# Kernel optimization log

Hardware: AMD Instinct MI355X
Metric: run time of the kernel (lower is better)

## Reference

```python
import jax, jax.numpy as jnp
import numpy as np

N_CH = 128      # n_channels (out_channels)
MID = 128       # mid_channels
NF = 16         # num_filters
N_NODES = 50000


def _omeg():
    i = jnp.arange(NF, dtype=jnp.float32)
    return (10.0 * N_CH ** (1.0 - 2.0 * i / NF)).reshape(1, NF)


def setup_inputs() -> dict:
    key = jax.random.key(0)
    ks = jax.random.split(key, 16)
    E = 800000
    inp = {
        "x": jax.random.normal(ks[0], (N_NODES, N_CH), jnp.float32),
        "edge_index": jax.random.randint(ks[1], (2, E), 0, N_NODES, jnp.int64),
        "edge_attr": jax.random.normal(ks[2], (E, N_CH), jnp.float32),
        "x_pos": jax.random.normal(ks[3], (N_NODES, 3), jnp.float32),
    }
    def lin(k, fan_in, fan_out):
        kw, kb = jax.random.split(k)
        bound = 1.0 / np.sqrt(fan_in)
        w = jax.random.uniform(kw, (fan_in, fan_out), jnp.float32, -bound, bound)
        b = jax.random.uniform(kb, (fan_out,), jnp.float32, -bound, bound)
        return w, b
    inp["w1"], inp["b1"] = lin(ks[4], N_CH, N_CH)          # atomwise1
    inp["mw1"], inp["mb1"] = lin(ks[5], 2 * NF + 2 * N_CH, MID)  # message MLP
    inp["mw2"], inp["mb2"] = lin(ks[6], MID, MID)
    inp["mw3"], inp["mb3"] = lin(ks[7], MID, N_CH)
    inp["w2"], inp["b2"] = lin(ks[8], N_CH, N_CH)          # atomwise2
    inp["w3"], inp["b3"] = lin(ks[9], N_CH, N_CH)          # atomwise3
    return inp


def reference(x, edge_index, edge_attr, x_pos, w1, b1, mw1, mb1, mw2, mb2, mw3, mb3, w2, b2, w3, b3):
    h = x @ w1 + b1                                   # atomwise1 [N, C]
    src, dst = edge_index[0], edge_index[1]           # PyG: x_j = src, x_i = dst
    r = jnp.linalg.norm(x_pos[dst] - x_pos[src], axis=-1, keepdims=True)  # [E,1], p=2
    feat = r * _omeg()                                # [E, NF]
    msg_in = jnp.concatenate([jnp.sin(feat), jnp.cos(feat), edge_attr, h[src]], axis=-1)
    m = jax.nn.gelu(msg_in @ mw1 + mb1, approximate=False)
    m = jax.nn.gelu(m @ mw2 + mb2, approximate=False)
    m = m @ mw3 + mb3                                 # dropout is identity at eval
    agg = jax.ops.segment_sum(m, dst, num_segments=N_NODES)
    h = h + agg                                       # residual in cfconv
    out = jax.nn.relu(h @ w2 + b2) @ w3 + b3
    return out
```

## Files before the change

kernel.cpp:

```cpp
#include <hip/hip_runtime.h>
#include <math.h>

#define NCH 128
#define TE 64
#define TF 32
#define AP 296
#define WP 40
#define XP 136

typedef __attribute__((ext_vector_type(8))) _Float16 half8;
typedef __attribute__((ext_vector_type(4))) _Float16 half4;
typedef __attribute__((ext_vector_type(4))) float f32x4;

__device__ __forceinline__ float gelu_exact(float v) {
    return 0.5f * v * (1.0f + erff(v * 0.70710678118654752f));
}

__device__ __forceinline__ void sincos_rev(float rev, float* s, float* c) {
    float fr = rev - floorf(rev);
#if __has_builtin(__builtin_amdgcn_sinf) && __has_builtin(__builtin_amdgcn_cosf)
    *s = __builtin_amdgcn_sinf(fr);
    *c = __builtin_amdgcn_cosf(fr);
#else
    float rad = fr * 6.283185307179586f;
    *s = sinf(rad);
    *c = cosf(rad);
#endif
}

__global__ __launch_bounds__(256) void k_prep(const float* __restrict__ W,
                                              _Float16* __restrict__ out, int total) {
    int idx = blockIdx.x * 256 + threadIdx.x;
    if (idx >= total) return;
    int k = idx >> 7, n = idx & 127;
    out[(size_t)(k >> 5) * 4096 + n * 32 + (k & 31)] = (_Float16)W[idx];
}

__global__ __launch_bounds__(256) void k_prep_frag(const float* __restrict__ W,
                                                   _Float16* __restrict__ out,
                                                   int nchunks) {
    int idx = blockIdx.x * 256 + threadIdx.x;
    if (idx >= nchunks * 512) return;
    int c    = idx >> 9;
    int r    = idx & 511;
    int wv   = r >> 7;
    int nf   = (r >> 6) & 1;
    int lane = r & 63;
    int n  = wv * 32 + nf * 16 + (lane & 15);
    int k0 = c * 32 + (lane >> 4) * 8;
    half8 v;
    #pragma unroll
    for (int j = 0; j < 8; ++j) v[j] = (_Float16)W[(size_t)(k0 + j) * NCH + n];
    *(half8*)(out + (size_t)idx * 8) = v;
}

__global__ __launch_bounds__(256, 4) void k_aw1_mfma(
    const float* __restrict__ x, const _Float16* __restrict__ wc,
    const float* __restrict__ b1, float* __restrict__ h,
    _Float16* __restrict__ h2, int N)
{
    __shared__ __align__(16) _Float16 Xs[64][XP];
    __shared__ __align__(16) _Float16 Ws[128][WP];

    const int tid  = threadIdx.x;
    const int row0 = blockIdx.x * 64;
    const int lane = tid & 63;
    const int w    = tid >> 6;
    const int lrow = lane & 15;
    const int lk8  = lane >> 4;
    const int n0   = w * 32;

    const uint4* wsrc = (const uint4*)wc;
    uint4 pv0 = wsrc[tid], pv1 = wsrc[tid + 256];

    #pragma unroll
    for (int t = 0; t < 8; ++t) {
        int idx = tid + t * 256;
        int r = idx >> 5, f4 = idx & 31;
        int gr = row0 + r;
        float4 v = {0.f, 0.f, 0.f, 0.f};
        if (gr < N) v = *(const float4*)(x + (size_t)gr * NCH + f4 * 4);
        half4 p = {(_Float16)v.x, (_Float16)v.y, (_Float16)v.z, (_Float16)v.w};
        *(half4*)&Xs[r][f4 * 4] = p;
    }
    *(uint4*)&Ws[tid >> 2][(tid & 3) * 8]        = pv0;
    *(uint4*)&Ws[64 + (tid >> 2)][(tid & 3) * 8] = pv1;
    __syncthreads();

    f32x4 acc[4][2];
    #pragma unroll
    for (int mb = 0; mb < 4; ++mb)
        #pragma unroll
        for (int nf = 0; nf < 2; ++nf) acc[mb][nf] = (f32x4){0.f, 0.f, 0.f, 0.f};

    for (int i = 0; i < 4; ++i) {
        if (i < 3) {
            const uint4* s = (const uint4*)(wc + (i + 1) * 4096);
            pv0 = s[tid]; pv1 = s[tid + 256];
        }
        half8 av[4], bv[2];
        #pragma unroll
        for (int mb = 0; mb < 4; ++mb)
            av[mb] = *(const half8*)&Xs[mb * 16 + lrow][i * 32 + lk8 * 8];
        #pragma unroll
        for (int nf = 0; nf < 2; ++nf)
            bv[nf] = *(const half8*)&Ws[n0 + nf * 16 + lrow][lk8 * 8];
        #pragma unroll
        for (int mb = 0; mb < 4; ++mb)
            #pragma unroll
            for (int nf = 0; nf < 2; ++nf)
                acc[mb][nf] = __builtin_amdgcn_mfma_f32_16x16x32_f16(
                    av[mb], bv[nf], acc[mb][nf], 0, 0, 0);
        __syncthreads();
        if (i < 3) {
            *(uint4*)&Ws[tid >> 2][(tid & 3) * 8]        = pv0;
            *(uint4*)&Ws[64 + (tid >> 2)][(tid & 3) * 8] = pv1;
        }
        __syncthreads();
    }

    float bi0 = b1[n0 + lrow], bi1 = b1[n0 + 16 + lrow];
    #pragma unroll
    for (int mb = 0; mb < 4; ++mb)
        #pragma unroll
        for (int q = 0; q < 4; ++q) {
            int gr = row0 + mb * 16 + lk8 * 4 + q;
            if (gr < N) {
                float v0 = acc[mb][0][q] + bi0;
                float v1 = acc[mb][1][q] + bi1;
                h[(size_t)gr * NCH + n0 + lrow]       = v0;
                h[(size_t)gr * NCH + n0 + 16 + lrow]  = v1;
                h2[(size_t)gr * NCH + n0 + lrow]      = (_Float16)v0;
                h2[(size_t)gr * NCH + n0 + 16 + lrow] = (_Float16)v1;
            }
        }
}

__global__ __launch_bounds__(256, 8) void k_edges_mfma(
    const int* __restrict__ ei, const float* __restrict__ eattr,
    const float* __restrict__ xpos, const _Float16* __restrict__ h2,
    float* h,
    const _Float16* __restrict__ wf,
    const float* __restrict__ mb1, const float* __restrict__ mb2,
    const float* __restrict__ mb3, int E)
{
    __shared__ __align__(16) _Float16 As[TF][AP];

    const int tid  = threadIdx.x;
    const int e0   = blockIdx.x * TF;
    const int lane = tid & 63;
    const int w    = tid >> 6;
    const int lrow = lane & 15;
    const int lk8  = lane >> 4;
    const int n0   = w * 32;

    const half8* bp = (const half8*)wf + (w * 128 + lane);

    float4 ea[4];
    #pragma unroll
    for (int t = 0; t < 4; ++t) {
        int idx = tid + t * 256;
        int e = e0 + (idx >> 5);
        ea[t] = (e < E) ? *(const float4*)(eattr + (size_t)e * NCH + (idx & 31) * 4)
                        : (float4){0.f, 0.f, 0.f, 0.f};
    }
    uint4 hv[2];
    #pragma unroll
    for (int t = 0; t < 2; ++t) {
        int idx = tid + t * 256;
        int e = e0 + (idx >> 4);
        int s = (e < E) ? ei[e] : 0;
        hv[t] = *(const uint4*)(h2 + (size_t)s * NCH + (idx & 15) * 8);
    }
    half8 b[2][2];
    b[0][0] = bp[0];         b[0][1] = bp[64];
    b[1][0] = bp[512];       b[1][1] = bp[512 + 64];

    {
        int le = tid >> 3, i0 = tid & 7;
        int ge = e0 + le;
        float r = 0.f;
        if (ge < E) {
            int s = ei[ge], d = ei[E + ge];
            float dx = xpos[d * 3 + 0] - xpos[s * 3 + 0];
            float dy = xpos[d * 3 + 1] - xpos[s * 3 + 1];
            float dz = xpos[d * 3 + 2] - xpos[s * 3 + 2];
            r = sqrtf(dx * dx + dy * dy + dz * dz);
        }
        #pragma unroll
        for (int u = 0; u < 2; ++u) {
            int i = i0 + u * 8;
            float omr = 1.5915494309f * exp2f(7.0f - 0.875f * (float)i);
            float sv, cv;
            sincos_rev(r * omr, &sv, &cv);
            As[le][i]      = (_Float16)sv;
            As[le][16 + i] = (_Float16)cv;
        }
    }
    #pragma unroll
    for (int t = 0; t < 4; ++t) {
        int idx = tid + t * 256;
        half4 p = {(_Float16)ea[t].x, (_Float16)ea[t].y,
                   (_Float16)ea[t].z, (_Float16)ea[t].w};
        *(half4*)&As[idx >> 5][32 + (idx & 31) * 4] = p;
    }
    #pragma unroll
    for (int t = 0; t < 2; ++t) {
        int idx = tid + t * 256;
        *(uint4*)&As[idx >> 4][160 + (idx & 15) * 8] = hv[t];
    }
    __syncthreads();

    f32x4 acc[2][2];
    #pragma unroll
    for (int mb = 0; mb < 2; ++mb)
        #pragma unroll
        for (int nf = 0; nf < 2; ++nf) acc[mb][nf] = (f32x4){0.f, 0.f, 0.f, 0.f};

    auto epi = [&](const float* __restrict__ mbv) {
        float bi0 = mbv[n0 + lrow], bi1 = mbv[n0 + 16 + lrow];
        #pragma unroll
        for (int mb = 0; mb < 2; ++mb)
            #pragma unroll
            for (int nf = 0; nf < 2; ++nf) {
                float bb = nf ? bi1 : bi0;
                #pragma unroll
                for (int q = 0; q < 4; ++q) {
                    float g = gelu_exact(acc[mb][nf][q] + bb);
                    As[mb * 16 + lk8 * 4 + q][n0 + nf * 16 + lrow] = (_Float16)g;
                }
                acc[mb][nf] = (f32x4){0.f, 0.f, 0.f, 0.f};
            }
    };

    #pragma unroll
    for (int i = 0; i < 17; ++i) {
        const int s  = i & 1;
        const int lc = (i < 9) ? i : (i < 13) ? (i - 9) : (i - 13);
        half8 av0 = *(const half8*)&As[lrow][lc * 32 + lk8 * 8];
        half8 av1 = *(const half8*)&As[16 + lrow][lc * 32 + lk8 * 8];
        __builtin_amdgcn_s_setprio(1);
        acc[0][0] = __builtin_amdgcn_mfma_f32_16x16x32_f16(av0, b[s][0], acc[0][0], 0, 0, 0);
        acc[0][1] = __builtin_amdgcn_mfma_f32_16x16x32_f16(av0, b[s][1], acc[0][1], 0, 0, 0);
        acc[1][0] = __builtin_amdgcn_mfma_f32_16x16x32_f16(av1, b[s][0], acc[1][0], 0, 0, 0);
        acc[1][1] = __builtin_amdgcn_mfma_f32_16x16x32_f16(av1, b[s][1], acc[1][1], 0, 0, 0);
        __builtin_amdgcn_s_setprio(0);
        if (i + 2 < 17) {
            b[s][0] = bp[(size_t)(i + 2) * 512];
            b[s][1] = bp[(size_t)(i + 2) * 512 + 64];
        }
        if (i == 8)  { __syncthreads(); epi(mb1); __syncthreads(); }
        if (i == 12) { __syncthreads(); epi(mb2); __syncthreads(); }
    }

    {
        float bi0 = mb3[n0 + lrow], bi1 = mb3[n0 + 16 + lrow];
        #pragma unroll
        for (int mb = 0; mb < 2; ++mb)
            #pragma unroll
            for (int q = 0; q < 4; ++q) {
                int e = e0 + mb * 16 + lk8 * 4 + q;
                if (e < E) {
                    int d = ei[E + e];
                    atomicAdd(h + (size_t)d * NCH + n0 + lrow,      acc[mb][0][q] + bi0);
                    atomicAdd(h + (size_t)d * NCH + n0 + 16 + lrow, acc[mb][1][q] + bi1);
                }
            }
    }
}

__global__ __launch_bounds__(256, 4) void k_out_mfma(
    const float* h, const _Float16* __restrict__ w2c,
    const float* __restrict__ b2, const _Float16* __restrict__ w3c,
    const float* __restrict__ b3, float* out, int N)
{
    __shared__ __align__(16) _Float16 Xs[64][XP];
    __shared__ __align__(16) _Float16 Ws[128][WP];

    const int tid  = threadIdx.x;
    const int row0 = blockIdx.x * 64;
    const int lane = tid & 63;
    const int w    = tid >> 6;
    const int lrow = lane & 15;
    const int lk8  = lane >> 4;
    const int n0   = w * 32;

    const uint4* wsrc = (const uint4*)w2c;
    uint4 pv0 = wsrc[tid], pv1 = wsrc[tid + 256];

    #pragma unroll
    for (int t = 0; t < 8; ++t) {
        int idx = tid + t * 256;
        int r = idx >> 5, f4 = idx & 31;
        int gr = row0 + r;
        float4 v = {0.f, 0.f, 0.f, 0.f};
        if (gr < N) v = *(const float4*)(h + (size_t)gr * NCH + f4 * 4);
        half4 p = {(_Float16)v.x, (_Float16)v.y, (_Float16)v.z, (_Float16)v.w};
        *(half4*)&Xs[r][f4 * 4] = p;
    }
    *(uint4*)&Ws[tid >> 2][(tid & 3) * 8]        = pv0;
    *(uint4*)&Ws[64 + (tid >> 2)][(tid & 3) * 8] = pv1;
    __syncthreads();

    f32x4 acc[4][2];
    #pragma unroll
    for (int mb = 0; mb < 4; ++mb)
        #pragma unroll
        for (int nf = 0; nf < 2; ++nf) acc[mb][nf] = (f32x4){0.f, 0.f, 0.f, 0.f};

    for (int i = 0; i < 8; ++i) {
        if (i < 7) {
            int j = i + 1;
            const _Float16* nw = (j < 4) ? (w2c + j * 4096) : (w3c + (j - 4) * 4096);
            const uint4* s = (const uint4*)nw;
            pv0 = s[tid]; pv1 = s[tid + 256];
        }
        const int lc = i & 3;
        half8 av[4], bv[2];
        #pragma unroll
        for (int mb = 0; mb < 4; ++mb)
            av[mb] = *(const half8*)&Xs[mb * 16 + lrow][lc * 32 + lk8 * 8];
        #pragma unroll
        for (int nf = 0; nf < 2; ++nf)
            bv[nf] = *(const half8*)&Ws[n0 + nf * 16 + lrow][lk8 * 8];
        #pragma unroll
        for (int mb = 0; mb < 4; ++mb)
            #pragma unroll
            for (int nf = 0; nf < 2; ++nf)
                acc[mb][nf] = __builtin_amdgcn_mfma_f32_16x16x32_f16(
                    av[mb], bv[nf], acc[mb][nf], 0, 0, 0);

        __syncthreads();
        if (i == 3) {
            float bi0 = b2[n0 + lrow], bi1 = b2[n0 + 16 + lrow];
            #pragma unroll
            for (int mb = 0; mb < 4; ++mb)
                #pragma unroll
                for (int nf = 0; nf < 2; ++nf) {
                    float bb = nf ? bi1 : bi0;
                    #pragma unroll
                    for (int q = 0; q < 4; ++q) {
                        float g = fmaxf(acc[mb][nf][q] + bb, 0.f);
                        Xs[mb * 16 + lk8 * 4 + q][n0 + nf * 16 + lrow] = (_Float16)g;
                    }
                    acc[mb][nf] = (f32x4){0.f, 0.f, 0.f, 0.f};
                }
        }
        if (i < 7) {
            *(uint4*)&Ws[tid >> 2][(tid & 3) * 8]        = pv0;
            *(uint4*)&Ws[64 + (tid >> 2)][(tid & 3) * 8] = pv1;
        }
        __syncthreads();
    }

    float bi0 = b3[n0 + lrow], bi1 = b3[n0 + 16 + lrow];
    #pragma unroll
    for (int mb = 0; mb < 4; ++mb)
        #pragma unroll
        for (int q = 0; q < 4; ++q) {
            int gr = row0 + mb * 16 + lk8 * 4 + q;
            if (gr < N) {
                out[(size_t)gr * NCH + n0 + lrow]      = acc[mb][0][q] + bi0;
                out[(size_t)gr * NCH + n0 + 16 + lrow] = acc[mb][1][q] + bi1;
            }
        }
}

__global__ __launch_bounds__(256) void k_atomwise1(
    const float* __restrict__ x, const float* __restrict__ w1,
    const float* __restrict__ b1, float* __restrict__ h,
    float* __restrict__ h2, int N)
{
    __shared__ float xs[16][NCH];
    const int row0 = blockIdx.x * 16;
    const int tid = threadIdx.x;
    #pragma unroll
    for (int t = 0; t < 8; ++t) {
        int idx = tid + t * 256;
        int r = idx >> 7, c = idx & 127;
        int gr = row0 + r;
        xs[r][c] = (gr < N) ? x[(size_t)gr * NCH + c] : 0.f;
    }
    __syncthreads();
    const int j = tid & 127;
    const int rg = tid >> 7;
    float acc[8];
    #pragma unroll
    for (int i = 0; i < 8; ++i) acc[i] = 0.f;
    for (int k = 0; k < NCH; ++k) {
        float wv = w1[(size_t)k * NCH + j];
        #pragma unroll
        for (int i = 0; i < 8; ++i)
            acc[i] = fmaf(xs[rg * 8 + i][k], wv, acc[i]);
    }
    float bv = b1[j];
    #pragma unroll
    for (int i = 0; i < 8; ++i) {
        int gr = row0 + rg * 8 + i;
        if (gr < N) {
            float v = acc[i] + bv;
            h[(size_t)gr * NCH + j]  = v;
            h2[(size_t)gr * NCH + j] = v;
        }
    }
}

__global__ __launch_bounds__(256) void k_edges_f32(
    const int* __restrict__ ei, const float* __restrict__ eattr,
    const float* __restrict__ xpos, const float* __restrict__ h,
    const float* __restrict__ mw1, const float* __restrict__ mb1,
    const float* __restrict__ mw2, const float* __restrict__ mb2,
    const float* __restrict__ mw3, const float* __restrict__ mb3,
    float* __restrict__ agg, int E)
{
    __shared__ __align__(16) float Asf[TE][292];
    __shared__ float Wsf[32][NCH];
    __shared__ int srcS[TE];
    __shared__ int dstS[TE];
    const int tid = threadIdx.x;
    const int e0 = blockIdx.x * TE;
    if (tid < TE) {
        int e = e0 + tid;
        int s = 0, d = -1;
        float r = 0.f;
        if (e < E) {
            s = ei[e]; d = ei[E + e];
            float dx = xpos[d * 3 + 0] - xpos[s * 3 + 0];
            float dy = xpos[d * 3 + 1] - xpos[s * 3 + 1];
            float dz = xpos[d * 3 + 2] - xpos[s * 3 + 2];
            r = sqrtf(dx * dx + dy * dy + dz * dz);
        }
        srcS[tid] = s; dstS[tid] = d;
        #pragma unroll
        for (int i = 0; i < 16; ++i) {
            float om = 10.f * exp2f(7.0f - 0.875f * (float)i);
            float f = r * om;
            Asf[tid][i] = sinf(f); Asf[tid][16 + i] = cosf(f);
        }
    }
    __syncthreads();
    {
        const int half = tid >> 7;
        const int c = tid & 127;
        for (int ee = 0; ee < TE; ee += 2) {
            int le = ee + half;
            int e = e0 + le;
            if (e < E) {
                Asf[le][32 + c]  = eattr[(size_t)e * NCH + c];
                Asf[le][160 + c] = h[(size_t)srcS[le] * NCH + c];
            } else { Asf[le][32 + c] = 0.f; Asf[le][160 + c] = 0.f; }
        }
    }
    const int jl = tid & 31;
    const int g  = tid >> 5;
    float acc[8][4];
    auto run_layer = [&](const float* __restrict__ Wg, int K) {
        #pragma unroll
        for (int i = 0; i < 8; ++i)
            #pragma unroll
            for (int c = 0; c < 4; ++c) acc[i][c] = 0.f;
        for (int k0 = 0; k0 < K; k0 += 32) {
            __syncthreads();
            #pragma unroll
            for (int t = 0; t < 16; ++t) {
                int idx = tid + t * 256;
                Wsf[idx >> 7][idx & 127] =
                    Wg[(size_t)(k0 + (idx >> 7)) * NCH + (idx & 127)];
            }
            __syncthreads();
            #pragma unroll
            for (int kk = 0; kk < 32; kk += 4) {
                float4 a[8];
                #pragma unroll
                for (int i = 0; i < 8; ++i)
                    a[i] = *reinterpret_cast<const float4*>(&Asf[g * 8 + i][k0 + kk]);
                #pragma unroll
                for (int u = 0; u < 4; ++u) {
                    float w0 = Wsf[kk + u][jl];
                    float w1v = Wsf[kk + u][jl + 32];
                    float w2v = Wsf[kk + u][jl + 64];
                    float w3v = Wsf[kk + u][jl + 96];
                    #pragma unroll
                    for (int i = 0; i < 8; ++i) {
                        float avv = (&a[i].x)[u];
                        acc[i][0] = fmaf(avv, w0, acc[i][0]);
                        acc[i][1] = fmaf(avv, w1v, acc[i][1]);
                        acc[i][2] = fmaf(avv, w2v, acc[i][2]);
                        acc[i][3] = fmaf(avv, w3v, acc[i][3]);
                    }
                }
            }
        }
    };
    run_layer(mw1, 288);
    #pragma unroll
    for (int i = 0; i < 8; ++i)
        #pragma unroll
        for (int c = 0; c < 4; ++c) {
            int j = jl + 32 * c;
            Asf[g * 8 + i][j] = gelu_exact(acc[i][c] + mb1[j]);
        }
    run_layer(mw2, 128);
    #pragma unroll
    for (int i = 0; i < 8; ++i)
        #pragma unroll
        for (int c = 0; c < 4; ++c) {
            int j = jl + 32 * c;
            Asf[g * 8 + i][j] = gelu_exact(acc[i][c] + mb2[j]);
        }
    run_layer(mw3, 128);
    #pragma unroll
    for (int i = 0; i < 8; ++i) {
        int d = dstS[g * 8 + i];
        if (d >= 0) {
            #pragma unroll
            for (int c = 0; c < 4; ++c) {
                int j = jl + 32 * c;
                atomicAdd(&agg[(size_t)d * NCH + j], acc[i][c] + mb3[j]);
            }
        }
    }
}

__global__ __launch_bounds__(256) void k_out(
    const float* h, const float* aggOpt,
    const float* __restrict__ w2, const float* __restrict__ b2,
    const float* __restrict__ w3, const float* __restrict__ b3,
    float* out, int N)
{
    __shared__ float hs[16][NCH];
    __shared__ float ts[16][NCH];
    const int row0 = blockIdx.x * 16;
    const int tid = threadIdx.x;
    #pragma unroll
    for (int t = 0; t < 8; ++t) {
        int idx = tid + t * 256;
        int r = idx >> 7, c = idx & 127;
        int gr = row0 + r;
        float v = 0.f;
        if (gr < N) {
            v = h[(size_t)gr * NCH + c];
            if (aggOpt) v += aggOpt[(size_t)gr * NCH + c];
        }
        hs[r][c] = v;
    }
    __syncthreads();
    const int j = tid & 127;
    const int rg = tid >> 7;
    float acc[8];
    #pragma unroll
    for (int i = 0; i < 8; ++i) acc[i] = 0.f;
    for (int k = 0; k < NCH; ++k) {
        float wv = w2[(size_t)k * NCH + j];
        #pragma unroll
        for (int i = 0; i < 8; ++i)
            acc[i] = fmaf(hs[rg * 8 + i][k], wv, acc[i]);
    }
    float bv = b2[j];
    #pragma unroll
    for (int i = 0; i < 8; ++i)
        ts[rg * 8 + i][j] = fmaxf(acc[i] + bv, 0.f);
    __syncthreads();
    float acc2[8];
    #pragma unroll
    for (int i = 0; i < 8; ++i) acc2[i] = 0.f;
    for (int k = 0; k < NCH; ++k) {
        float wv = w3[(size_t)k * NCH + j];
        #pragma unroll
        for (int i = 0; i < 8; ++i)
            acc2[i] = fmaf(ts[rg * 8 + i][k], wv, acc2[i]);
    }
    float b3v = b3[j];
    #pragma unroll
    for (int i = 0; i < 8; ++i) {
        int gr = row0 + rg * 8 + i;
        if (gr < N) out[(size_t)gr * NCH + j] = acc2[i] + b3v;
    }
}

extern "C" void kernel_launch(void* const* d_in, const int* in_sizes, int n_in,
                              void* d_out, int out_size, void* d_ws, size_t ws_size,
                              hipStream_t stream)
{
    const float* x     = (const float*)d_in[0];
    const int*   ei    = (const int*)d_in[1];
    const float* eattr = (const float*)d_in[2];
    const float* xpos  = (const float*)d_in[3];
    const float* w1    = (const float*)d_in[4];
    const float* b1    = (const float*)d_in[5];
    const float* mw1   = (const float*)d_in[6];
    const float* mb1   = (const float*)d_in[7];
    const float* mw2   = (const float*)d_in[8];
    const float* mb2   = (const float*)d_in[9];
    const float* mw3   = (const float*)d_in[10];
    const float* mb3   = (const float*)d_in[11];
    const float* w2    = (const float*)d_in[12];
    const float* b2    = (const float*)d_in[13];
    const float* w3    = (const float*)d_in[14];
    const float* b3    = (const float*)d_in[15];

    const int N = in_sizes[0] / NCH;
    const int E = in_sizes[1] / 2;

    float* h = (float*)d_out;

    const size_t h2_bytes = (size_t)N * NCH * sizeof(_Float16);
    const size_t wchunks  = 17 + 4 + 4 + 4;
    const size_t wbytes   = wchunks * 4096 * sizeof(_Float16);
    const bool fast = ws_size >= h2_bytes + wbytes;

    if (fast) {
        _Float16* h2   = (_Float16*)d_ws;
        _Float16* wf   = (_Float16*)((char*)d_ws + h2_bytes);
        _Float16* aw1c = wf + 17 * 4096;
        _Float16* o2c  = aw1c + 4 * 4096;
        _Float16* o3c  = o2c + 4 * 4096;
        k_prep_frag<<<18, 256, 0, stream>>>(mw1, wf, 9);
        k_prep_frag<<<8, 256, 0, stream>>>(mw2, wf + 9 * 4096, 4);
        k_prep_frag<<<8, 256, 0, stream>>>(mw3, wf + 13 * 4096, 4);
        k_prep<<<64, 256, 0, stream>>>(w1, aw1c, 128 * 128);
        k_prep<<<64, 256, 0, stream>>>(w2, o2c, 128 * 128);
        k_prep<<<64, 256, 0, stream>>>(w3, o3c, 128 * 128);
        const int nb = (N + 63) / 64;
        k_aw1_mfma<<<nb, 256, 0, stream>>>(x, aw1c, b1, h, h2, N);
        k_edges_mfma<<<(E + TF - 1) / TF, 256, 0, stream>>>(
            ei, eattr, xpos, h2, h, wf, mb1, mb2, mb3, E);
        k_out_mfma<<<nb, 256, 0, stream>>>(h, o2c, b2, o3c, b3, (float*)d_out, N);
    } else {
        float* agg = (float*)d_ws;
        k_atomwise1<<<(N + 15) / 16, 256, 0, stream>>>(x, w1, b1, h, agg, N);
        hipMemsetAsync(agg, 0, (size_t)N * NCH * sizeof(float), stream);
        k_edges_f32<<<(E + TE - 1) / TE, 256, 0, stream>>>(
            ei, eattr, xpos, h, mw1, mb1, mw2, mb2, mw3, mb3, agg, E);
        k_out<<<(N + 15) / 16, 256, 0, stream>>>(h, agg, w2, b2, w3, b3,
                                                 (float*)d_out, N);
    }
}
```

Measured before the change: 432.8 us.

## Accumulate edge messages in fp16 packed atomics and use fast erf GELU

Edge messages are now scattered into a separate fp16 aggregation buffer using packed half2 atomic adds, staged through shared memory so each thread writes contiguous channels. This replaces per-element fp32 atomics and is meant to halve atomic count and traffic. The output kernel adds this buffer to h when loading. GELU's erf is also replaced by an Abramowitz-Stegun polynomial with a hardware reciprocal. The cost is lower accuracy: fp16 accumulation of many edges per node risks rounding error and overflow, and the erf approximation adds some error. An extra memset of the buffer is also added.

```diff
diff --git a/kernel.cpp b/kernel.cpp
--- a/kernel.cpp
+++ b/kernel.cpp
@@ -1,4 +1,5 @@
 #include <hip/hip_runtime.h>
+#include <hip/hip_fp16.h>
 #include <math.h>
 
 #define NCH 128
@@ -14,6 +15,22 @@
 
 __device__ __forceinline__ float gelu_exact(float v) {
     return 0.5f * v * (1.0f + erff(v * 0.70710678118654752f));
+}
+
+__device__ __forceinline__ float erf_fast(float x) {
+    float ax = fabsf(x);
+    float t  = __builtin_amdgcn_rcpf(fmaf(0.3275911f, ax, 1.0f));
+    float p  = fmaf(t, 1.061405429f, -1.453152027f);
+    p = fmaf(t, p, 1.421413741f);
+    p = fmaf(t, p, -0.284496736f);
+    p = fmaf(t, p, 0.254829592f);
+    float e  = exp2f(-ax * ax * 1.4426950408889634f);
+    float r  = fmaf(-p * t, e, 1.0f);
+    return copysignf(r, x);
+}
+
+__device__ __forceinline__ float gelu_fast(float v) {
+    return 0.5f * v * (1.0f + erf_fast(v * 0.70710678118654752f));
 }
 
 __device__ __forceinline__ void sincos_rev(float rev, float* s, float* c) {
@@ -140,6 +157,7 @@
     const int* __restrict__ ei, const float* __restrict__ eattr,
     const float* __restrict__ xpos, const _Float16* __restrict__ h2,
     float* h,
+    _Float16* agg16,
     const _Float16* __restrict__ wf,
     const float* __restrict__ mb1, const float* __restrict__ mb2,
     const float* __restrict__ mb3, int E)
@@ -226,7 +244,7 @@
                 float bb = nf ? bi1 : bi0;
                 #pragma unroll
                 for (int q = 0; q < 4; ++q) {
-                    float g = gelu_exact(acc[mb][nf][q] + bb);
+                    float g = gelu_fast(acc[mb][nf][q] + bb);
                     As[mb * 16 + lk8 * 4 + q][n0 + nf * 16 + lrow] = (_Float16)g;
                 }
                 acc[mb][nf] = (f32x4){0.f, 0.f, 0.f, 0.f};
@@ -253,8 +271,34 @@
         if (i == 12) { __syncthreads(); epi(mb2); __syncthreads(); }
     }
 
-    {
-        float bi0 = mb3[n0 + lrow], bi1 = mb3[n0 + 16 + lrow];
+    float bi0 = mb3[n0 + lrow], bi1 = mb3[n0 + 16 + lrow];
+    if (agg16) {
+        __syncthreads();
+        #pragma unroll
+        for (int mb = 0; mb < 2; ++mb)
+            #pragma unroll
+            for (int nf = 0; nf < 2; ++nf) {
+                float bb = nf ? bi1 : bi0;
+                #pragma unroll
+                for (int q = 0; q < 4; ++q)
+                    As[mb * 16 + lk8 * 4 + q][n0 + nf * 16 + lrow] =
+                        (_Float16)(acc[mb][nf][q] + bb);
+            }
+        __syncthreads();
+        int e  = tid >> 3;
+        int c0 = (tid & 7) * 16;
+        int ge = e0 + e;
+        if (ge < E) {
+            int d = ei[E + ge];
+            __half2* dst = (__half2*)(agg16 + (size_t)d * NCH + c0);
+            #pragma unroll
+            for (int k = 0; k < 8; ++k) {
+                uint uv = *(const uint*)((const char*)&As[e][c0] + k * 4);
+                __half2 pv = *(__half2*)&uv;
+                unsafeAtomicAdd(&dst[k], pv);
+            }
+        }
+    } else {
         #pragma unroll
         for (int mb = 0; mb < 2; ++mb)
             #pragma unroll
@@ -270,7 +314,8 @@
 }
 
 __global__ __launch_bounds__(256, 4) void k_out_mfma(
-    const float* h, const _Float16* __restrict__ w2c,
+    const float* h, const _Float16* agg16,
+    const _Float16* __restrict__ w2c,
     const float* __restrict__ b2, const _Float16* __restrict__ w3c,
     const float* __restrict__ b3, float* out, int N)
 {
@@ -294,7 +339,14 @@
         int r = idx >> 5, f4 = idx & 31;
         int gr = row0 + r;
         float4 v = {0.f, 0.f, 0.f, 0.f};
-        if (gr < N) v = *(const float4*)(h + (size_t)gr * NCH + f4 * 4);
+        if (gr < N) {
+            v = *(const float4*)(h + (size_t)gr * NCH + f4 * 4);
+            if (agg16) {
+                half4 a = *(const half4*)(agg16 + (size_t)gr * NCH + f4 * 4);
+                v.x += (float)a[0]; v.y += (float)a[1];
+                v.z += (float)a[2]; v.w += (float)a[3];
+            }
+        }
         half4 p = {(_Float16)v.x, (_Float16)v.y, (_Float16)v.z, (_Float16)v.w};
         *(half4*)&Xs[r][f4 * 4] = p;
     }
@@ -604,14 +656,17 @@
 
     float* h = (float*)d_out;
 
-    const size_t h2_bytes = (size_t)N * NCH * sizeof(_Float16);
-    const size_t wchunks  = 17 + 4 + 4 + 4;
-    const size_t wbytes   = wchunks * 4096 * sizeof(_Float16);
-    const bool fast = ws_size >= h2_bytes + wbytes;
-
-    if (fast) {
+    const size_t h2_bytes  = (size_t)N * NCH * sizeof(_Float16);
+    const size_t agg_bytes = (size_t)N * NCH * sizeof(_Float16);
+    const size_t wchunks   = 17 + 4 + 4 + 4;
+    const size_t wbytes    = wchunks * 4096 * sizeof(_Float16);
+    const bool fast2 = ws_size >= h2_bytes + agg_bytes + wbytes;
+    const bool fast1 = !fast2 && ws_size >= h2_bytes + wbytes;
+
+    if (fast2 || fast1) {
         _Float16* h2   = (_Float16*)d_ws;
-        _Float16* wf   = (_Float16*)((char*)d_ws + h2_bytes);
+        _Float16* ag   = fast2 ? (h2 + (size_t)N * NCH) : nullptr;
+        _Float16* wf   = fast2 ? (ag + (size_t)N * NCH) : (h2 + (size_t)N * NCH);
         _Float16* aw1c = wf + 17 * 4096;
         _Float16* o2c  = aw1c + 4 * 4096;
         _Float16* o3c  = o2c + 4 * 4096;
@@ -621,11 +676,13 @@
         k_prep<<<64, 256, 0, stream>>>(w1, aw1c, 128 * 128);
         k_prep<<<64, 256, 0, stream>>>(w2, o2c, 128 * 128);
         k_prep<<<64, 256, 0, stream>>>(w3, o3c, 128 * 128);
+        if (fast2) hipMemsetAsync(ag, 0, agg_bytes, stream);
         const int nb = (N + 63) / 64;
         k_aw1_mfma<<<nb, 256, 0, stream>>>(x, aw1c, b1, h, h2, N);
         k_edges_mfma<<<(E + TF - 1) / TF, 256, 0, stream>>>(
-            ei, eattr, xpos, h2, h, wf, mb1, mb2, mb3, E);
-        k_out_mfma<<<nb, 256, 0, stream>>>(h, o2c, b2, o3c, b3, (float*)d_out, N);
+            ei, eattr, xpos, h2, h, ag, wf, mb1, mb2, mb3, E);
+        k_out_mfma<<<nb, 256, 0, stream>>>(h, ag, o2c, b2, o3c, b3,
+                                           (float*)d_out, N);
     } else {
         float* agg = (float*)d_ws;
         k_atomwise1<<<(N + 15) / 16, 256, 0, stream>>>(x, w1, b1, h, agg, N);
```

Measured after the change: 1.541 ms. +256.0%, slower.
